# Kernel tuning notes

Hardware: AMD Instinct MI355X
Metric: run time of the kernel (lower is better)

The kernel has to match this reference:

```python
import jax, jax.numpy as jnp
import numpy as np

B, S, R, C_IN = 1, 1024, 512, 256   # batch, n_seq (MSA rows), n_res, rep1d_extra_feat
H, CH = 8, 32                       # num_heads, attention_num_c (H*CH == C_IN)


def setup_inputs() -> dict:
    key = jax.random.key(0)
    ks = jax.random.split(key, 7)
    scale = 0.02
    return {
        "x1d": jax.random.normal(ks[0], (B, S, R, C_IN), jnp.float32),
        "mask": jnp.ones((B, S, R), jnp.float32),
        "ln_scale": jnp.ones((C_IN,), jnp.float32),
        "ln_bias": jnp.zeros((C_IN,), jnp.float32),
        "Wq": jax.random.normal(ks[1], (C_IN, H * CH), jnp.float32) * scale,
        "Wk": jax.random.normal(ks[2], (C_IN, CH), jnp.float32) * scale,
        "Wv": jax.random.normal(ks[3], (C_IN, CH), jnp.float32) * scale,
        "Wg": jax.random.normal(ks[4], (C_IN, H * CH), jnp.float32) * scale,
        "bg": jnp.zeros((H * CH,), jnp.float32),
        "Wf": jax.random.normal(ks[5], (H * CH, C_IN), jnpp := jnp.float32) * scale if False else jax.random.normal(ks[5], (H * CH, C_IN), jnp.float32) * scale,
        "bf": jnp.zeros((C_IN,), jnp.float32),
    }


def reference(x1d, mask, ln_scale, ln_bias, Wq, Wk, Wv, Wg, bg, Wf, bf):
    # transpose so attention runs over the MSA-row (column) axis
    x = jnp.swapaxes(x1d, -2, -3)          # [B, R, S, C_IN]
    m = jnp.swapaxes(mask, -1, -2)         # [B, R, S]
    # LayerNorm (eps matches torch default 1e-5)
    mu = jnp.mean(x, axis=-1, keepdims=True)
    var = jnp.mean((x - mu) ** 2, axis=-1, keepdims=True)
    xn = (x - mu) * jax.lax.rsqrt(var + 1e-5) * ln_scale + ln_bias
    # masked mean over rows -> global query
    q_avg = jnp.sum(xn * m[..., None], axis=-2) / (jnp.sum(m, axis=-1)[..., None] + 1e-10)  # [B,R,C_IN]
    att_bias = (1e9 * (m - 1.0))[..., None, :]                         # [B,R,1,S]
    q = (q_avg @ Wq).reshape(*q_avg.shape[:-1], H, CH) * (CH ** -0.5)  # [B,R,H,CH]
    k = xn @ Wk                                                        # [B,R,S,CH]
    v = xn @ Wv                                                        # [B,R,S,CH]
    gate = jax.nn.sigmoid(xn @ Wg + bg).reshape(*xn.shape[:-1], H, CH)  # [B,R,S,H,CH]
    w = jax.nn.softmax(jnp.einsum('brhc,brsc->brhs', q, k) + att_bias, axis=-1)  # [B,R,H,S]
    o = jnp.einsum('brhs,brsc->brhc', w, v)                            # [B,R,H,CH]
    o = o[..., None, :, :] * gate                                      # [B,R,S,H,CH]
    out = o.reshape(*o.shape[:-2], H * CH) @ Wf + bf                   # [B,R,S,C_IN]
    return jnp.swapaxes(out, -2, -3)                                   # [B,S,R,C_IN]
```

## Files before the change

kernel.cpp:

```cpp
#include <hip/hip_runtime.h>
#include <hip/hip_bf16.h>

#define S_DIM 1024
#define R_DIM 512
#define C_DIM 256
#define BS 64
#define SB (S_DIM / BS)

#define XN_OFF (16u << 20)
#define XN_BYTES (512ull * 1024ull * 256ull * 2ull)

typedef __attribute__((ext_vector_type(8))) short short8;
typedef __attribute__((ext_vector_type(8))) unsigned short ushort8v;
typedef __attribute__((ext_vector_type(4))) unsigned short ushort4v;
typedef __attribute__((ext_vector_type(4))) float floatx4;

__device__ inline float bf2f(unsigned short u) {
    return __uint_as_float(((unsigned int)u) << 16);
}
__device__ inline unsigned short f2bf(float f) {
    unsigned int x = __float_as_uint(f);
    unsigned int r = ((x >> 16) & 1u) + 0x7fffu;
    return (unsigned short)((x + r) >> 16);
}

__device__ inline float fast_rcp(float x) {
    float r;
    asm volatile("v_rcp_f32 %0, %1" : "=v"(r) : "v"(x));
    return r;
}

__device__ inline void async16nt(unsigned short* lds, const unsigned short* g) {
    __builtin_amdgcn_global_load_lds(
        (const __attribute__((address_space(1))) void*)g,
        (__attribute__((address_space(3))) void*)lds, 16, 0, 2);
}

__global__ __launch_bounds__(256) void prep_kernel(
        const float* __restrict__ Wk, const float* __restrict__ Wv,
        const float* __restrict__ Wg, const float* __restrict__ Wf,
        unsigned short* __restrict__ wgT, unsigned short* __restrict__ wfhi,
        unsigned short* __restrict__ wflo, unsigned short* __restrict__ wkvT) {
    int b = blockIdx.x;
    int k = threadIdx.x;
    wgT[b * 256 + k] = f2bf(Wg[k * 256 + b]);
    float w = Wf[k * 256 + b];
    unsigned short hi = f2bf(w);
    wfhi[b * 256 + k] = hi;
    wflo[b * 256 + k] = f2bf(w - bf2f(hi));
    if (b < 64) {
        float t = (b < 32) ? Wk[k * 32 + b] : Wv[k * 32 + (b - 32)];
        wkvT[b * 256 + k] = f2bf(t);
    }
}

__global__ __launch_bounds__(256, 4) void k1a_kernel(
        const float* __restrict__ x, const float* __restrict__ lns,
        const float* __restrict__ lnb, unsigned short* __restrict__ xnws) {
    const int t = threadIdx.x;
    const int row = t >> 3;
    const int q = t & 7;
    const size_t base = ((size_t)blockIdx.x * 32 + row) * 256 + q * 32;
    const floatx4* gp = reinterpret_cast<const floatx4*>(x + base);
    floatx4 v[8];
    float sum = 0.f, sq = 0.f;
#pragma unroll
    for (int i = 0; i < 8; i++) {
        v[i] = gp[i];
        sum += v[i][0] + v[i][1] + v[i][2] + v[i][3];
        sq  += v[i][0] * v[i][0] + v[i][1] * v[i][1]
             + v[i][2] * v[i][2] + v[i][3] * v[i][3];
    }
    sum += __shfl_xor(sum, 1); sq += __shfl_xor(sq, 1);
    sum += __shfl_xor(sum, 2); sq += __shfl_xor(sq, 2);
    sum += __shfl_xor(sum, 4); sq += __shfl_xor(sq, 4);
    float mu = sum * (1.f / 256.f);
    float var = sq * (1.f / 256.f) - mu * mu;
    float rs = rsqrtf(var + 1e-5f);
    const floatx4* sp = reinterpret_cast<const floatx4*>(lns + q * 32);
    const floatx4* bp = reinterpret_cast<const floatx4*>(lnb + q * 32);
    unsigned short* gw = xnws + base;
#pragma unroll
    for (int i = 0; i < 8; i += 2) {
        floatx4 g0 = sp[i],     b0 = bp[i];
        floatx4 g1 = sp[i + 1], b1 = bp[i + 1];
        ushort8v u;
        u[0] = f2bf((v[i][0]     - mu) * rs * g0[0] + b0[0]);
        u[1] = f2bf((v[i][1]     - mu) * rs * g0[1] + b0[1]);
        u[2] = f2bf((v[i][2]     - mu) * rs * g0[2] + b0[2]);
        u[3] = f2bf((v[i][3]     - mu) * rs * g0[3] + b0[3]);
        u[4] = f2bf((v[i + 1][0] - mu) * rs * g1[0] + b1[0]);
        u[5] = f2bf((v[i + 1][1] - mu) * rs * g1[1] + b1[1]);
        u[6] = f2bf((v[i + 1][2] - mu) * rs * g1[2] + b1[2]);
        u[7] = f2bf((v[i + 1][3] - mu) * rs * g1[3] + b1[3]);
        *reinterpret_cast<ushort8v*>(gw + i * 4) = u;
    }
}

__global__ __launch_bounds__(256, 4) void k1b_kernel(
        const unsigned short* __restrict__ xnws, const float* __restrict__ mask,
        const unsigned short* __restrict__ wkvT, unsigned short* __restrict__ kv,
        float* __restrict__ qsum, float* __restrict__ msum) {
    __shared__ unsigned short xn[64 * 256];
    __shared__ float mk[64];
    const int sblk = blockIdx.x, r = blockIdx.y;
    const int s0 = sblk * BS;
    const int t = threadIdx.x;
    const int w = t >> 6, l = t & 63;

    {
        const int c1 = l & 31;
        const int rh = l >> 5;
#pragma unroll
        for (int j = 0; j < 8; j++) {
            int row = w * 16 + 2 * j + rh;
            size_t src = ((size_t)(s0 + row) * R_DIM + r) * C_DIM
                         + (size_t)((c1 ^ (row & 7)) * 8);
            async16nt(xn + (w * 16 + 2 * j) * 256, xnws + src);
        }
    }
    if (t < 64) mk[t] = mask[(size_t)(s0 + t) * R_DIM + r];
    __syncthreads();

    const int lr = l & 15, lk4 = l >> 4;
    const int sw = lr & 7;
    floatx4 acc[4] = {};
#pragma unroll
    for (int kk = 0; kk < 256; kk += 32) {
        const int ch = (((kk >> 3) + lk4) ^ sw) * 8;
        short8 a = *reinterpret_cast<const short8*>(xn + (w * 16 + lr) * 256 + ch);
#pragma unroll
        for (int n = 0; n < 4; n++) {
            short8 b = *reinterpret_cast<const short8*>(wkvT + (n * 16 + lr) * 256 + kk + lk4 * 8);
            acc[n] = __builtin_amdgcn_mfma_f32_16x16x32_bf16(a, b, acc[n], 0, 0, 0);
        }
    }
    unsigned short* kvp = kv + ((size_t)r * S_DIM + s0) * 64;
#pragma unroll
    for (int n = 0; n < 4; n++) {
        int col = n * 16 + lr;
#pragma unroll
        for (int i = 0; i < 4; i++) {
            int row = w * 16 + lk4 * 4 + i;
            kvp[(size_t)row * 64 + col] = f2bf(acc[n][i]);
        }
    }
    {
        const int c = t;
        const int chi = c >> 3, clo = c & 7;
        float cs = 0.f;
#pragma unroll 8
        for (int row = 0; row < 64; row++)
            cs += bf2f(xn[row * 256 + ((chi ^ (row & 7)) * 8 + clo)]) * mk[row];
        qsum[((size_t)r * SB + sblk) * 256 + c] = cs;
    }
    if (t < 64) {
        float m = mk[t];
#pragma unroll
        for (int off = 32; off; off >>= 1) m += __shfl_xor(m, off);
        if (t == 0) msum[r * SB + sblk] = m;
    }
}

__global__ __launch_bounds__(256, 4) void k1_old_kernel(
        const float* __restrict__ x, const float* __restrict__ mask,
        const float* __restrict__ lns, const float* __restrict__ lnb,
        const unsigned short* __restrict__ wkvT, unsigned short* __restrict__ kv,
        float* __restrict__ qsum, float* __restrict__ msum) {
    __shared__ unsigned short xn[64 * 264];
    __shared__ float mk[64];
    const int sblk = blockIdx.x, r = blockIdx.y;
    const int s0 = sblk * BS;
    const int t = threadIdx.x;
    {
        const int row = t >> 2;
        const int q = t & 3;
        const size_t base = ((size_t)(s0 + row) * R_DIM + r) * C_DIM + q * 64;
        const floatx4* gp = reinterpret_cast<const floatx4*>(x + base);
        floatx4 v[16];
        float sum = 0.f, sq = 0.f;
#pragma unroll
        for (int i = 0; i < 16; i++) {
            v[i] = gp[i];
            sum += v[i][0] + v[i][1] + v[i][2] + v[i][3];
            sq  += v[i][0] * v[i][0] + v[i][1] * v[i][1] + v[i][2] * v[i][2] + v[i][3] * v[i][3];
        }
        sum += __shfl_xor(sum, 1); sq += __shfl_xor(sq, 1);
        sum += __shfl_xor(sum, 2); sq += __shfl_xor(sq, 2);
        float mu = sum * (1.f / 256.f);
        float var = sq * (1.f / 256.f) - mu * mu;
        float rs = rsqrtf(var + 1e-5f);
        const floatx4* sp = reinterpret_cast<const floatx4*>(lns + q * 64);
        const floatx4* bp = reinterpret_cast<const floatx4*>(lnb + q * 64);
        unsigned short* wp = xn + row * 264 + q * 64;
#pragma unroll
        for (int i = 0; i < 16; i += 2) {
            floatx4 g0 = sp[i],     b0 = bp[i];
            floatx4 g1 = sp[i + 1], b1 = bp[i + 1];
            ushort8v u;
            u[0] = f2bf((v[i][0]     - mu) * rs * g0[0] + b0[0]);
            u[1] = f2bf((v[i][1]     - mu) * rs * g0[1] + b0[1]);
            u[2] = f2bf((v[i][2]     - mu) * rs * g0[2] + b0[2]);
            u[3] = f2bf((v[i][3]     - mu) * rs * g0[3] + b0[3]);
            u[4] = f2bf((v[i + 1][0] - mu) * rs * g1[0] + b1[0]);
            u[5] = f2bf((v[i + 1][1] - mu) * rs * g1[1] + b1[1]);
            u[6] = f2bf((v[i + 1][2] - mu) * rs * g1[2] + b1[2]);
            u[7] = f2bf((v[i + 1][3] - mu) * rs * g1[3] + b1[3]);
            *reinterpret_cast<ushort8v*>(wp + i * 4) = u;
        }
    }
    if (t < 64) mk[t] = mask[(size_t)(s0 + t) * R_DIM + r];
    __syncthreads();

    const int w = t >> 6, l = t & 63;
    const int lr = l & 15, lk = (l >> 4) * 8;
    floatx4 acc[4] = {};
    const unsigned short* arow = xn + (w * 16 + lr) * 264;
#pragma unroll
    for (int kk = 0; kk < 256; kk += 32) {
        short8 a = *reinterpret_cast<const short8*>(arow + kk + lk);
#pragma unroll
        for (int n = 0; n < 4; n++) {
            short8 b = *reinterpret_cast<const short8*>(wkvT + (n * 16 + lr) * 256 + kk + lk);
            acc[n] = __builtin_amdgcn_mfma_f32_16x16x32_bf16(a, b, acc[n], 0, 0, 0);
        }
    }
    unsigned short* kvp = kv + ((size_t)r * S_DIM + s0) * 64;
#pragma unroll
    for (int n = 0; n < 4; n++) {
        int col = n * 16 + lr;
#pragma unroll
        for (int i = 0; i < 4; i++) {
            int row = w * 16 + (l >> 4) * 4 + i;
            kvp[(size_t)row * 64 + col] = f2bf(acc[n][i]);
        }
    }
    float cs = 0.f;
    const int c = t;
#pragma unroll 8
    for (int row = 0; row < 64; row++) cs += bf2f(xn[row * 264 + c]) * mk[row];
    qsum[((size_t)r * SB + sblk) * 256 + c] = cs;
    if (t < 64) {
        float m = mk[t];
#pragma unroll
        for (int off = 32; off; off >>= 1) m += __shfl_xor(m, off);
        if (t == 0) msum[r * SB + sblk] = m;
    }
}

__global__ __launch_bounds__(256) void k2_kernel(
        const float* __restrict__ mask, const float* __restrict__ Wq,
        const float* __restrict__ qsum, const float* __restrict__ msum,
        const unsigned short* __restrict__ kv, float* __restrict__ oout) {
    __shared__ float qavg[256];
    __shared__ float qh[256];
    __shared__ float lg[8][1024];
    __shared__ unsigned short vt[256 * 36];
    const int r = blockIdx.x;
    const int t = threadIdx.x;

    float ms = 0.f;
#pragma unroll
    for (int i = 0; i < SB; i++) ms += msum[r * SB + i];
    float inv = 1.f / (ms + 1e-10f);
    float qs = 0.f;
#pragma unroll
    for (int i = 0; i < SB; i++) qs += qsum[((size_t)r * SB + i) * 256 + t];
    qavg[t] = qs * inv;
    __syncthreads();

    float accq = 0.f;
#pragma unroll 8
    for (int c = 0; c < 256; c++) accq += qavg[c] * Wq[c * 256 + t];
    qh[t] = accq * 0.17677669529663687f;
    __syncthreads();

    const unsigned short* kvr = kv + (size_t)r * S_DIM * 64;
#pragma unroll
    for (int i = 0; i < 4; i++) {
        int s = i * 256 + t;
        float bias = 1e9f * (mask[(size_t)s * R_DIM + r] - 1.f);
        const unsigned int* kp = reinterpret_cast<const unsigned int*>(kvr + (size_t)s * 64);
        float kvals[32];
#pragma unroll
        for (int j = 0; j < 16; j++) {
            unsigned int u = kp[j];
            kvals[2 * j]     = __uint_as_float(u << 16);
            kvals[2 * j + 1] = __uint_as_float(u & 0xffff0000u);
        }
#pragma unroll
        for (int h = 0; h < 8; h++) {
            float d = 0.f;
#pragma unroll
            for (int ch = 0; ch < 32; ch++) d += qh[h * 32 + ch] * kvals[ch];
            lg[h][s] = d + bias;
        }
    }
    __syncthreads();

    {
        const int h = t >> 5;
        const int g = t & 31;
        float* lrow = &lg[h][0];
        float mx = -1e30f;
#pragma unroll
        for (int j = 0; j < 32; j++)
            mx = fmaxf(mx, lrow[g * 32 + ((j + g) & 31)]);
#pragma unroll
        for (int off = 16; off; off >>= 1) mx = fmaxf(mx, __shfl_xor(mx, off));
        float vals[32];
        float sm = 0.f;
#pragma unroll
        for (int j = 0; j < 32; j++) {
            float e = __expf(lrow[g * 32 + ((j + g) & 31)] - mx);
            vals[j] = e;
            sm += e;
        }
#pragma unroll
        for (int off = 16; off; off >>= 1) sm += __shfl_xor(sm, off);
        float isv = 1.f / sm;
#pragma unroll
        for (int j = 0; j < 32; j++)
            lrow[g * 32 + ((j + g) & 31)] = vals[j] * isv;
    }
    __syncthreads();

    const int h = t >> 5, ch = t & 31;
    float o = 0.f;
    for (int st = 0; st < 4; st++) {
        __syncthreads();
        {
            const unsigned short* src = kvr + ((size_t)(st * 256 + t)) * 64 + 32;
            ushort4v* dst = reinterpret_cast<ushort4v*>(vt + t * 36);
#pragma unroll
            for (int j = 0; j < 8; j++)
                dst[j] = *reinterpret_cast<const ushort4v*>(src + 4 * j);
        }
        __syncthreads();
#pragma unroll 8
        for (int sl = 0; sl < 256; sl++)
            o += lg[h][sl + st * 256] * bf2f(vt[sl * 36 + ch]);
    }
    oout[r * 256 + t] = o;
}

__global__ __launch_bounds__(256, 4) void k3r_kernel(
        const float* __restrict__ x, const float* __restrict__ lns,
        const float* __restrict__ lnb, const unsigned short* __restrict__ wgT,
        const unsigned short* __restrict__ wfhi, const unsigned short* __restrict__ wflo,
        const float* __restrict__ oin, const float* __restrict__ bg,
        const float* __restrict__ bfv, float* __restrict__ out) {
    __shared__ unsigned short xa[64 * 264];
    const int sblk = blockIdx.x, r = blockIdx.y;
    const int s0 = sblk * BS;
    const int t = threadIdx.x;
    {
        const int row = t >> 2;
        const int q = t & 3;
        const size_t base = ((size_t)(s0 + row) * R_DIM + r) * C_DIM + q * 64;
        const floatx4* gp = reinterpret_cast<const floatx4*>(x + base);
        floatx4 v[16];
        float sum = 0.f, sq = 0.f;
#pragma unroll
        for (int i = 0; i < 16; i++) {
            v[i] = gp[i];
            sum += v[i][0] + v[i][1] + v[i][2] + v[i][3];
            sq  += v[i][0] * v[i][0] + v[i][1] * v[i][1] + v[i][2] * v[i][2] + v[i][3] * v[i][3];
        }
        sum += __shfl_xor(sum, 1); sq += __shfl_xor(sq, 1);
        sum += __shfl_xor(sum, 2); sq += __shfl_xor(sq, 2);
        float mu = sum * (1.f / 256.f);
        float var = sq * (1.f / 256.f) - mu * mu;
        float rs = rsqrtf(var + 1e-5f);
        const floatx4* sp = reinterpret_cast<const floatx4*>(lns + q * 64);
        const floatx4* bp = reinterpret_cast<const floatx4*>(lnb + q * 64);
        unsigned short* wp = xa + row * 264 + q * 64;
#pragma unroll
        for (int i = 0; i < 16; i += 2) {
            floatx4 g0 = sp[i],     b0 = bp[i];
            floatx4 g1 = sp[i + 1], b1 = bp[i + 1];
            ushort8v u;
            u[0] = f2bf((v[i][0]     - mu) * rs * g0[0] + b0[0]);
            u[1] = f2bf((v[i][1]     - mu) * rs * g0[1] + b0[1]);
            u[2] = f2bf((v[i][2]     - mu) * rs * g0[2] + b0[2]);
            u[3] = f2bf((v[i][3]     - mu) * rs * g0[3] + b0[3]);
            u[4] = f2bf((v[i + 1][0] - mu) * rs * g1[0] + b1[0]);
            u[5] = f2bf((v[i + 1][1] - mu) * rs * g1[1] + b1[1]);
            u[6] = f2bf((v[i + 1][2] - mu) * rs * g1[2] + b1[2]);
            u[7] = f2bf((v[i + 1][3] - mu) * rs * g1[3] + b1[3]);
            *reinterpret_cast<ushort8v*>(wp + i * 4) = u;
        }
    }
    __syncthreads();

    const int w = t >> 6, l = t & 63;
    const int lr = l & 15, lk4 = (l >> 4);
    const int colbase = w * 64;

    float bgv[4], ov[4];
#pragma unroll
    for (int n = 0; n < 4; n++) {
        int col = colbase + n * 16 + lr;
        bgv[n] = bg[col];
        ov[n] = oin[r * 256 + col];
    }

    floatx4 acc[4][4] = {};
#pragma unroll
    for (int kk = 0; kk < 256; kk += 32) {
        short8 a[4];
#pragma unroll
        for (int m = 0; m < 4; m++)
            a[m] = *reinterpret_cast<const short8*>(xa + (m * 16 + lr) * 264 + kk + lk4 * 8);
#pragma unroll
        for (int n = 0; n < 4; n++) {
            short8 b = *reinterpret_cast<const short8*>(wgT + (size_t)(colbase + n * 16 + lr) * 256 + kk + lk4 * 8);
#pragma unroll
            for (int m = 0; m < 4; m++)
                acc[m][n] = __builtin_amdgcn_mfma_f32_16x16x32_bf16(a[m], b, acc[m][n], 0, 0, 0);
        }
    }
    __syncthreads();

#pragma unroll
    for (int m = 0; m < 4; m++) {
#pragma unroll
        for (int n = 0; n < 4; n++) {
            int col = colbase + n * 16 + lr;
#pragma unroll
            for (int i = 0; i < 4; i++) {
                int row = m * 16 + lk4 * 4 + i;
                float e = __expf(-(acc[m][n][i] + bgv[n]));
                float g = fast_rcp(1.f + e);
                xa[row * 264 + col] = f2bf(g * ov[n]);
            }
        }
    }
    __syncthreads();

    floatx4 acc2[4][4] = {};
#pragma unroll
    for (int kk = 0; kk < 256; kk += 32) {
        short8 ah[4];
#pragma unroll
        for (int m = 0; m < 4; m++)
            ah[m] = *reinterpret_cast<const short8*>(xa + (m * 16 + lr) * 264 + kk + lk4 * 8);
#pragma unroll
        for (int n = 0; n < 4; n++) {
            const size_t boff = (size_t)(colbase + n * 16 + lr) * 256 + kk + lk4 * 8;
            short8 bh = *reinterpret_cast<const short8*>(wfhi + boff);
            short8 bl = *reinterpret_cast<const short8*>(wflo + boff);
#pragma unroll
            for (int m = 0; m < 4; m++) {
                acc2[m][n] = __builtin_amdgcn_mfma_f32_16x16x32_bf16(ah[m], bh, acc2[m][n], 0, 0, 0);
                acc2[m][n] = __builtin_amdgcn_mfma_f32_16x16x32_bf16(ah[m], bl, acc2[m][n], 0, 0, 0);
            }
        }
    }

#pragma unroll
    for (int n = 0; n < 4; n++) {
        int col = colbase + n * 16 + lr;
        float bfc = bfv[col];
#pragma unroll
        for (int m = 0; m < 4; m++) {
#pragma unroll
            for (int i = 0; i < 4; i++) {
                int row = m * 16 + lk4 * 4 + i;
                out[((size_t)(s0 + row) * R_DIM + r) * C_DIM + col] = acc2[m][n][i] + bfc;
            }
        }
    }
}

__global__ __launch_bounds__(256, 2) void k3c_kernel(
        const unsigned short* __restrict__ xnws, const unsigned short* __restrict__ wgT,
        const unsigned short* __restrict__ wfhi, const unsigned short* __restrict__ wflo,
        const float* __restrict__ oin, const float* __restrict__ bg,
        const float* __restrict__ bfv, float* __restrict__ out) {
    __shared__ unsigned short xa[2][64 * 256];
    const int sblk = blockIdx.x, r = blockIdx.y;
    const int s0 = sblk * 128;
    const int t = threadIdx.x;
    const int w = t >> 6, l = t & 63;

    {
        const int c1 = l & 31;
        const int rh = l >> 5;
#pragma unroll
        for (int T = 0; T < 2; T++)
#pragma unroll
            for (int j = 0; j < 8; j++) {
                int row = w * 16 + 2 * j + rh;
                size_t src = ((size_t)(s0 + T * 64 + row) * R_DIM + r) * C_DIM
                             + (size_t)((c1 ^ (row & 7)) * 8);
                async16nt(&xa[T][(w * 16 + 2 * j) * 256], xnws + src);
            }
    }

    const int lr = l & 15, lk4 = (l >> 4);
    const int colbase = w * 64;
    const int sw = lr & 7;
    const int c0 = colbase + lk4 * 4;

    floatx4 bg4[4], ov4[4];
    float bfc[4];
#pragma unroll
    for (int n = 0; n < 4; n++) {
        bg4[n] = *reinterpret_cast<const floatx4*>(bg + c0 + n * 16);
        ov4[n] = *reinterpret_cast<const floatx4*>(oin + r * 256 + c0 + n * 16);
        bfc[n] = bfv[colbase + n * 16 + lr];
    }
    __syncthreads();

    floatx4 acc[2][4][4] = {};
    {
        const unsigned short* wgb = wgT + (size_t)(colbase + lr) * 256 + lk4 * 8;
        short8 cw[4], nw[4];
#pragma unroll
        for (int n = 0; n < 4; n++)
            cw[n] = *reinterpret_cast<const short8*>(wgb + n * 4096);
#pragma unroll
        for (int kk = 0; kk < 256; kk += 32) {
            if (kk < 224) {
#pragma unroll
                for (int n = 0; n < 4; n++)
                    nw[n] = *reinterpret_cast<const short8*>(wgb + n * 4096 + kk + 32);
            }
            const int ch = (((kk >> 3) + lk4) ^ sw) * 8;
#pragma unroll
            for (int T = 0; T < 2; T++) {
                short8 a[4];
#pragma unroll
                for (int m = 0; m < 4; m++)
                    a[m] = *reinterpret_cast<const short8*>(&xa[T][(m * 16 + lr) * 256 + ch]);
#pragma unroll
                for (int n = 0; n < 4; n++)
#pragma unroll
                    for (int m = 0; m < 4; m++)
                        acc[T][m][n] = __builtin_amdgcn_mfma_f32_16x16x32_bf16(cw[n], a[m], acc[T][m][n], 0, 0, 0);
            }
            if (kk < 224) {
#pragma unroll
                for (int n = 0; n < 4; n++) cw[n] = nw[n];
            }
        }
    }
    __syncthreads();

#pragma unroll
    for (int T = 0; T < 2; T++)
#pragma unroll
    for (int m = 0; m < 4; m++) {
        const int row = m * 16 + lr;
        unsigned short* rowp = &xa[T][row * 256];
#pragma unroll
        for (int n = 0; n < 4; n++) {
            const int cb = c0 + n * 16;
            ushort4v pk;
#pragma unroll
            for (int i = 0; i < 4; i++) {
                float e = __expf(-(acc[T][m][n][i] + ((const float*)&bg4[n])[i]));
                float g = fast_rcp(1.f + e);
                pk[i] = f2bf(g * ((const float*)&ov4[n])[i]);
            }
            const int dst = (((cb >> 3) ^ sw) * 8) + (cb & 7);
            *reinterpret_cast<ushort4v*>(rowp + dst) = pk;
        }
    }
    __syncthreads();

    floatx4 acc2[2][4][4] = {};
    {
        const unsigned short* whb = wfhi + (size_t)(colbase + lr) * 256 + lk4 * 8;
        const unsigned short* wlb = wflo + (size_t)(colbase + lr) * 256 + lk4 * 8;
        short8 chw[4], clw[4], nhw[4], nlw[4];
#pragma unroll
        for (int n = 0; n < 4; n++) {
            chw[n] = *reinterpret_cast<const short8*>(whb + n * 4096);
            clw[n] = *reinterpret_cast<const short8*>(wlb + n * 4096);
        }
#pragma unroll
        for (int kk = 0; kk < 256; kk += 32) {
            if (kk < 224) {
#pragma unroll
                for (int n = 0; n < 4; n++) {
                    nhw[n] = *reinterpret_cast<const short8*>(whb + n * 4096 + kk + 32);
                    nlw[n] = *reinterpret_cast<const short8*>(wlb + n * 4096 + kk + 32);
                }
            }
            const int ch = (((kk >> 3) + lk4) ^ sw) * 8;
#pragma unroll
            for (int T = 0; T < 2; T++) {
                short8 ah[4];
#pragma unroll
                for (int m = 0; m < 4; m++)
                    ah[m] = *reinterpret_cast<const short8*>(&xa[T][(m * 16 + lr) * 256 + ch]);
#pragma unroll
                for (int n = 0; n < 4; n++)
#pragma unroll
                    for (int m = 0; m < 4; m++) {
                        acc2[T][m][n] = __builtin_amdgcn_mfma_f32_16x16x32_bf16(ah[m], chw[n], acc2[T][m][n], 0, 0, 0);
                        acc2[T][m][n] = __builtin_amdgcn_mfma_f32_16x16x32_bf16(ah[m], clw[n], acc2[T][m][n], 0, 0, 0);
                    }
            }
            if (kk < 224) {
#pragma unroll
                for (int n = 0; n < 4; n++) { chw[n] = nhw[n]; clw[n] = nlw[n]; }
            }
        }
    }

#pragma unroll
    for (int T = 0; T < 2; T++)
#pragma unroll
    for (int n = 0; n < 4; n++) {
        int col = colbase + n * 16 + lr;
#pragma unroll
        for (int m = 0; m < 4; m++) {
#pragma unroll
            for (int i = 0; i < 4; i++) {
                int row = T * 64 + m * 16 + lk4 * 4 + i;
                out[((size_t)(s0 + row) * R_DIM + r) * C_DIM + col] = acc2[T][m][n][i] + bfc[n];
            }
        }
    }
}

extern "C" void kernel_launch(void* const* d_in, const int* in_sizes, int n_in,
                              void* d_out, int out_size, void* d_ws, size_t ws_size,
                              hipStream_t stream) {
    const float* x1   = (const float*)d_in[0];
    const float* mask = (const float*)d_in[1];
    const float* lns  = (const float*)d_in[2];
    const float* lnb  = (const float*)d_in[3];
    const float* Wq   = (const float*)d_in[4];
    const float* Wk   = (const float*)d_in[5];
    const float* Wv   = (const float*)d_in[6];
    const float* Wg   = (const float*)d_in[7];
    const float* bg   = (const float*)d_in[8];
    const float* Wf   = (const float*)d_in[9];
    const float* bfv  = (const float*)d_in[10];

    char* ws = (char*)d_ws;
    unsigned short* wgT  = (unsigned short*)(ws);
    unsigned short* wfhi = (unsigned short*)(ws + 131072);
    unsigned short* wflo = (unsigned short*)(ws + 262144);
    unsigned short* wkvT = (unsigned short*)(ws + 393216);
    float* qsum = (float*)(ws + 425984);
    float* msum = (float*)(ws + 425984 + 8388608);
    float* oo   = (float*)(ws + 425984 + 8388608 + 32768);
    unsigned short* xnws = (unsigned short*)(ws + XN_OFF);
    unsigned short* kv = (unsigned short*)d_out;
    float* out = (float*)d_out;

    const bool big_ws = ws_size >= (size_t)XN_OFF + (size_t)XN_BYTES;

    prep_kernel<<<256, 256, 0, stream>>>(Wk, Wv, Wg, Wf, wgT, wfhi, wflo, wkvT);
    if (big_ws) {
        k1a_kernel<<<(S_DIM * R_DIM) / 32, 256, 0, stream>>>(x1, lns, lnb, xnws);
        k1b_kernel<<<dim3(SB, R_DIM), 256, 0, stream>>>(xnws, mask, wkvT, kv, qsum, msum);
        k2_kernel<<<R_DIM, 256, 0, stream>>>(mask, Wq, qsum, msum, kv, oo);
        k3c_kernel<<<dim3(SB / 2, R_DIM), 256, 0, stream>>>(xnws, wgT, wfhi, wflo, oo, bg, bfv, out);
    } else {
        k1_old_kernel<<<dim3(SB, R_DIM), 256, 0, stream>>>(x1, mask, lns, lnb, wkvT, kv, qsum, msum);
        k2_kernel<<<R_DIM, 256, 0, stream>>>(mask, Wq, qsum, msum, kv, oo);
        k3r_kernel<<<dim3(SB, R_DIM), 256, 0, stream>>>(x1, lns, lnb, wgT, wfhi, wflo, oo, bg, bfv, out);
    }
}
```

Baseline: 771.1 us.

## Split k3c work across 8 waves with 32-column slices per wave

The fused gate/output-projection kernel now launches 512 threads (8 waves), and each wave owns 32 output columns instead of 64. Accumulator arrays halve, and the register double-buffered weight prefetch is replaced by per-iteration loads, which cuts register pressure so more waves can be resident (launch bounds 512,4). The cost is less latency hiding on weight loads and more LDS A-fragment reads per output, since each A fragment now serves fewer MFMAs.

```diff
diff --git a/kernel.cpp b/kernel.cpp
--- a/kernel.cpp
+++ b/kernel.cpp
@@ -473,7 +473,7 @@
     }
 }
 
-__global__ __launch_bounds__(256, 2) void k3c_kernel(
+__global__ __launch_bounds__(512, 4) void k3c_kernel(
         const unsigned short* __restrict__ xnws, const unsigned short* __restrict__ wgT,
         const unsigned short* __restrict__ wfhi, const unsigned short* __restrict__ wflo,
         const float* __restrict__ oin, const float* __restrict__ bg,
@@ -490,43 +490,38 @@
 #pragma unroll
         for (int T = 0; T < 2; T++)
 #pragma unroll
-            for (int j = 0; j < 8; j++) {
-                int row = w * 16 + 2 * j + rh;
+            for (int j = 0; j < 4; j++) {
+                int row = w * 8 + 2 * j + rh;
                 size_t src = ((size_t)(s0 + T * 64 + row) * R_DIM + r) * C_DIM
                              + (size_t)((c1 ^ (row & 7)) * 8);
-                async16nt(&xa[T][(w * 16 + 2 * j) * 256], xnws + src);
+                async16nt(&xa[T][(w * 8 + 2 * j) * 256], xnws + src);
             }
     }
 
     const int lr = l & 15, lk4 = (l >> 4);
-    const int colbase = w * 64;
+    const int colbase = w * 32;
     const int sw = lr & 7;
     const int c0 = colbase + lk4 * 4;
 
-    floatx4 bg4[4], ov4[4];
-    float bfc[4];
-#pragma unroll
-    for (int n = 0; n < 4; n++) {
+    floatx4 bg4[2], ov4[2];
+    float bfc[2];
+#pragma unroll
+    for (int n = 0; n < 2; n++) {
         bg4[n] = *reinterpret_cast<const floatx4*>(bg + c0 + n * 16);
         ov4[n] = *reinterpret_cast<const floatx4*>(oin + r * 256 + c0 + n * 16);
         bfc[n] = bfv[colbase + n * 16 + lr];
     }
     __syncthreads();
 
-    floatx4 acc[2][4][4] = {};
+    floatx4 acc[2][4][2] = {};
     {
         const unsigned short* wgb = wgT + (size_t)(colbase + lr) * 256 + lk4 * 8;
-        short8 cw[4], nw[4];
-#pragma unroll
-        for (int n = 0; n < 4; n++)
-            cw[n] = *reinterpret_cast<const short8*>(wgb + n * 4096);
 #pragma unroll
         for (int kk = 0; kk < 256; kk += 32) {
-            if (kk < 224) {
-#pragma unroll
-                for (int n = 0; n < 4; n++)
-                    nw[n] = *reinterpret_cast<const short8*>(wgb + n * 4096 + kk + 32);
-            }
+            short8 cw[2];
+#pragma unroll
+            for (int n = 0; n < 2; n++)
+                cw[n] = *reinterpret_cast<const short8*>(wgb + n * 4096 + kk);
             const int ch = (((kk >> 3) + lk4) ^ sw) * 8;
 #pragma unroll
             for (int T = 0; T < 2; T++) {
@@ -535,14 +530,10 @@
                 for (int m = 0; m < 4; m++)
                     a[m] = *reinterpret_cast<const short8*>(&xa[T][(m * 16 + lr) * 256 + ch]);
 #pragma unroll
-                for (int n = 0; n < 4; n++)
+                for (int n = 0; n < 2; n++)
 #pragma unroll
                     for (int m = 0; m < 4; m++)
                         acc[T][m][n] = __builtin_amdgcn_mfma_f32_16x16x32_bf16(cw[n], a[m], acc[T][m][n], 0, 0, 0);
-            }
-            if (kk < 224) {
-#pragma unroll
-                for (int n = 0; n < 4; n++) cw[n] = nw[n];
             }
         }
     }
@@ -555,7 +546,7 @@
         const int row = m * 16 + lr;
         unsigned short* rowp = &xa[T][row * 256];
 #pragma unroll
-        for (int n = 0; n < 4; n++) {
+        for (int n = 0; n < 2; n++) {
             const int cb = c0 + n * 16;
             ushort4v pk;
 #pragma unroll
@@ -570,24 +561,17 @@
     }
     __syncthreads();
 
-    floatx4 acc2[2][4][4] = {};
+    floatx4 acc2[2][4][2] = {};
     {
         const unsigned short* whb = wfhi + (size_t)(colbase + lr) * 256 + lk4 * 8;
         const unsigned short* wlb = wflo + (size_t)(colbase + lr) * 256 + lk4 * 8;
-        short8 chw[4], clw[4], nhw[4], nlw[4];
-#pragma unroll
-        for (int n = 0; n < 4; n++) {
-            chw[n] = *reinterpret_cast<const short8*>(whb + n * 4096);
-            clw[n] = *reinterpret_cast<const short8*>(wlb + n * 4096);
-        }
 #pragma unroll
         for (int kk = 0; kk < 256; kk += 32) {
-            if (kk < 224) {
-#pragma unroll
-                for (int n = 0; n < 4; n++) {
-                    nhw[n] = *reinterpret_cast<const short8*>(whb + n * 4096 + kk + 32);
-                    nlw[n] = *reinterpret_cast<const short8*>(wlb + n * 4096 + kk + 32);
-                }
+            short8 chw[2], clw[2];
+#pragma unroll
+            for (int n = 0; n < 2; n++) {
+                chw[n] = *reinterpret_cast<const short8*>(whb + n * 4096 + kk);
+                clw[n] = *reinterpret_cast<const short8*>(wlb + n * 4096 + kk);
             }
             const int ch = (((kk >> 3) + lk4) ^ sw) * 8;
 #pragma unroll
@@ -597,24 +581,20 @@
                 for (int m = 0; m < 4; m++)
                     ah[m] = *reinterpret_cast<const short8*>(&xa[T][(m * 16 + lr) * 256 + ch]);
 #pragma unroll
-                for (int n = 0; n < 4; n++)
+                for (int n = 0; n < 2; n++)
 #pragma unroll
                     for (int m = 0; m < 4; m++) {
                         acc2[T][m][n] = __builtin_amdgcn_mfma_f32_16x16x32_bf16(ah[m], chw[n], acc2[T][m][n], 0, 0, 0);
                         acc2[T][m][n] = __builtin_amdgcn_mfma_f32_16x16x32_bf16(ah[m], clw[n], acc2[T][m][n], 0, 0, 0);
                     }
             }
-            if (kk < 224) {
-#pragma unroll
-                for (int n = 0; n < 4; n++) { chw[n] = nhw[n]; clw[n] = nlw[n]; }
-            }
         }
     }
 
 #pragma unroll
     for (int T = 0; T < 2; T++)
 #pragma unroll
-    for (int n = 0; n < 4; n++) {
+    for (int n = 0; n < 2; n++) {
         int col = colbase + n * 16 + lr;
 #pragma unroll
         for (int m = 0; m < 4; m++) {
@@ -661,7 +641,7 @@
         k1a_kernel<<<(S_DIM * R_DIM) / 32, 256, 0, stream>>>(x1, lns, lnb, xnws);
         k1b_kernel<<<dim3(SB, R_DIM), 256, 0, stream>>>(xnws, mask, wkvT, kv, qsum, msum);
         k2_kernel<<<R_DIM, 256, 0, stream>>>(mask, Wq, qsum, msum, kv, oo);
-        k3c_kernel<<<dim3(SB / 2, R_DIM), 256, 0, stream>>>(xnws, wgT, wfhi, wflo, oo, bg, bfv, out);
+        k3c_kernel<<<dim3(SB / 2, R_DIM), 512, 0, stream>>>(xnws, wgT, wfhi, wflo, oo, bg, bfv, out);
     } else {
         k1_old_kernel<<<dim3(SB, R_DIM), 256, 0, stream>>>(x1, mask, lns, lnb, wkvT, kv, qsum, msum);
         k2_kernel<<<R_DIM, 256, 0, stream>>>(mask, Wq, qsum, msum, kv, oo);
```

Result: slower. 792.7 us (+2.8%).
